# Optimization experiments

Hardware: AMD Instinct MI355X
Metric: run time of the kernel (lower is better)

## Reference

```python
import jax, jax.numpy as jnp
import numpy as np


def _quat_raw_mul(a, b):
    aw, ax, ay, az = a[..., 0], a[..., 1], a[..., 2], a[..., 3]
    bw, bx, by, bz = b[..., 0], b[..., 1], b[..., 2], b[..., 3]
    ow = aw * bw - ax * bx - ay * by - az * bz
    ox = aw * bx + ax * bw + ay * bz - az * by
    oy = aw * by - ax * bz + ay * bw + az * bx
    oz = aw * bz + ax * by - ay * bx + az * bw
    return jnp.stack([ow, ox, oy, oz], axis=-1)


def _standardize(q):
    # pytorch3d.quaternion_multiply standardizes sign so w >= 0
    return jnp.where(q[..., :1] < 0, -q, q)


def _quat_apply(q, v):
    # rotate points v by unit quaternions q: q * (0, v) * conj(q), take imaginary part
    pv = jnp.concatenate([jnp.zeros_like(v[..., :1]), v], axis=-1)
    conj = q * jnp.asarray([1.0, -1.0, -1.0, -1.0], dtype=q.dtype)
    return _quat_raw_mul(_quat_raw_mul(q, pv), conj)[..., 1:]


def _axis_angle_to_quat(aa):
    # pytorch3d.axis_angle_to_quaternion with small-angle Taylor branch
    angle = jnp.linalg.norm(aa, axis=-1, keepdims=True)
    half = 0.5 * angle
    eps = 1e-6
    small = jnp.abs(angle) < eps
    safe_angle = jnp.where(small, jnp.ones_like(angle), angle)
    k = jnp.where(small, 0.5 - angle * angle / 48.0, jnp.sin(half) / safe_angle)
    return jnp.concatenate([jnp.cos(half), aa * k], axis=-1)


def _matrix_to_quat(M):
    # pytorch3d.matrix_to_quaternion (candidate-selection form), vectorized
    m00, m11, m22 = M[..., 0, 0], M[..., 1, 1], M[..., 2, 2]
    q_abs = jnp.sqrt(jax.nn.relu(jnp.stack([
        1.0 + m00 + m11 + m22,
        1.0 + m00 - m11 - m22,
        1.0 - m00 + m11 - m22,
        1.0 - m00 - m11 + m22], axis=-1)))
    c0 = jnp.stack([q_abs[..., 0] ** 2, M[..., 2, 1] - M[..., 1, 2], M[..., 0, 2] - M[..., 2, 0], M[..., 1, 0] - M[..., 0, 1]], axis=-1)
    c1 = jnp.stack([M[..., 2, 1] - M[..., 1, 2], q_abs[..., 1] ** 2, M[..., 1, 0] + M[..., 0, 1], M[..., 0, 2] + M[..., 2, 0]], axis=-1)
    c2 = jnp.stack([M[..., 0, 2] - M[..., 2, 0], M[..., 1, 0] + M[..., 0, 1], q_abs[..., 2] ** 2, M[..., 2, 1] + M[..., 1, 2]], axis=-1)
    c3 = jnp.stack([M[..., 1, 0] - M[..., 0, 1], M[..., 2, 0] + M[..., 0, 2], M[..., 2, 1] + M[..., 1, 2], q_abs[..., 3] ** 2], axis=-1)
    cands = jnp.stack([c0, c1, c2, c3], axis=-2)  # (..., 4 candidates, 4)
    flr = 0.1
    cands = cands / (2.0 * jnp.maximum(q_abs[..., None], flr))
    idx = jnp.argmax(q_abs, axis=-1)
    return jnp.take_along_axis(cands, idx[..., None, None], axis=-2)[..., 0, :]


def _or6d_to_quat(d6):
    a1, a2 = d6[..., :3], d6[..., 3:]
    b1 = a1 / jnp.linalg.norm(a1, axis=-1, keepdims=True)
    a2p = a2 - jnp.sum(b1 * a2, axis=-1, keepdims=True) * b1
    b2 = a2p / jnp.linalg.norm(a2p, axis=-1, keepdims=True)
    b3 = jnp.cross(b1, b2)
    M = jnp.stack([b1, b2, b3], axis=-2)  # (..., 3, 3)
    return _matrix_to_quat(M)


def setup_inputs() -> dict:
    key = jax.random.key(0)
    k1, k2, k3, k4 = jax.random.split(key, 4)
    N, T, J = 256, 1024, 24
    return {
        'root_rvel': jax.random.normal(k1, (N, T, 1, 1), dtype=jnp.float32),
        'local_pos': jax.random.normal(k2, (N, T + 1, J, 3), dtype=jnp.float32),
        'local_rot': jax.random.normal(k3, (N, T + 1, J, 6), dtype=jnp.float32),
        'root_vel': jax.random.normal(k4, (N, T, 1, 2), dtype=jnp.float32),
    }


def reference(root_rvel, local_pos, local_rot, root_vel):
    # cumulative root yaw angle with zero initial frame: (N, T+1, 1, 1)
    r = jnp.cumsum(root_rvel, axis=1)
    r = jnp.concatenate([jnp.zeros_like(r[:, :1]), r], axis=1)
    # axis-angle about Y axis -> quaternion (N, T+1, 1, 4)
    aa = r * jnp.asarray([0.0, 1.0, 0.0], dtype=r.dtype)
    rotation = _axis_angle_to_quat(aa)
    # local 6D rotations -> quaternions (N, T+1, J, 4)
    local_q = _or6d_to_quat(local_rot)
    global_rot = _standardize(_quat_raw_mul(rotation, local_q))
    relative_pos = _quat_apply(rotation, local_pos)
    # lift XZ hip velocity to 3D, rotate into world frame, integrate
    zeros_y = jnp.zeros_like(root_vel[..., :1])
    v3 = jnp.concatenate([root_vel[..., :1], zeros_y, root_vel[..., 1:]], axis=-1)  # (N,T,1,3)
    v3w = _quat_apply(rotation[:, :-1], v3)
    pos_xz = jnp.concatenate([jnp.zeros_like(v3w[:, :1]), jnp.cumsum(v3w, axis=1)], axis=1)  # (N,T+1,1,3)
    global_pos = relative_pos + pos_xz
    return global_pos, global_rot
```

## Files before the change

### kernel.cpp

```cpp
#include <hip/hip_runtime.h>

#define N_SEQ 256
#define T_LEN 1024
#define TP1   (T_LEN + 1)
#define J_NUM 24
#define SEQ_ITEMS (TP1 * J_NUM)
#define TOTAL_ITEMS (N_SEQ * SEQ_ITEMS)
#define GP_TOTAL (N_SEQ * TP1 * J_NUM * 3)

#define IPB 512
#define NBLOCKS_B (TOTAL_ITEMS / IPB)

__device__ __forceinline__ float block_scan_incl(float v, float* wsum, int tid) {
    const int lane = tid & 63;
    const int wid  = tid >> 6;
    #pragma unroll
    for (int off = 1; off < 64; off <<= 1) {
        float u = __shfl_up(v, off, 64);
        if (lane >= off) v += u;
    }
    if (lane == 63) wsum[wid] = v;
    __syncthreads();
    if (tid == 0) {
        float acc = 0.0f;
        #pragma unroll
        for (int i = 0; i < 16; ++i) { float t = wsum[i]; wsum[i] = acc; acc += t; }
    }
    __syncthreads();
    return v + wsum[wid];
}

extern "C" __global__ void __launch_bounds__(1024)
scan_kernel(const float* __restrict__ root_rvel,
            const float* __restrict__ root_vel,
            float4* __restrict__ ws4)
{
    const int n   = blockIdx.x;
    const int tid = threadIdx.x;

    __shared__ float  r_s[TP1];
    __shared__ float2 quat_s[TP1];
    __shared__ float  ws_a[16], ws_b[16], ws_c[16];

    {
        float v = root_rvel[n * T_LEN + tid];
        float incl = block_scan_incl(v, ws_a, tid);
        if (tid == 0) r_s[0] = 0.0f;
        r_s[tid + 1] = incl;
    }
    __syncthreads();

    for (int idx = tid; idx < TP1; idx += 1024) {
        float r     = r_s[idx];
        float angle = fabsf(r);
        float half  = 0.5f * angle;
        float k = (angle < 1e-6f) ? (0.5f - angle * angle * (1.0f / 48.0f))
                                  : (__builtin_sinf(half) / angle);
        quat_s[idx] = make_float2(__builtin_cosf(half), r * k);
    }
    __syncthreads();

    {
        float2 vel = ((const float2*)root_vel)[n * T_LEN + tid];
        float2 q   = quat_s[tid];
        float  w = q.x, y = q.y;
        float t1x = w * vel.x + y * vel.y;
        float t1z = w * vel.y - y * vel.x;
        float ax  = t1x * w + t1z * y;
        float az  = t1z * w - t1x * y;
        float ix = block_scan_incl(ax, ws_b, tid);
        float iz = block_scan_incl(az, ws_c, tid);
        float2 qn = quat_s[tid + 1];
        ws4[n * TP1 + tid + 1] = make_float4(qn.x, qn.y, ix, iz);
        if (tid == 0) ws4[n * TP1] = make_float4(1.0f, 0.0f, 0.0f, 0.0f);
    }
}

__device__ __forceinline__ void process_item(
    float a1x, float a1y, float a1z, float a2x, float a2y, float a2z,
    float vx,  float vy,  float vz,  float4 wq,
    float4* __restrict__ out_rot_addr, float* __restrict__ s_out3)
{
    const float w = wq.x, yq = wq.y;

    float inv1 = __builtin_amdgcn_rsqf(a1x * a1x + a1y * a1y + a1z * a1z);
    float b1x = a1x * inv1, b1y = a1y * inv1, b1z = a1z * inv1;
    float dp  = b1x * a2x + b1y * a2y + b1z * a2z;
    float px  = a2x - dp * b1x, py = a2y - dp * b1y, pz = a2z - dp * b1z;
    float inv2 = __builtin_amdgcn_rsqf(px * px + py * py + pz * pz);
    float b2x = px * inv2, b2y = py * inv2, b2z = pz * inv2;
    float b3x = b1y * b2z - b1z * b2y;
    float b3y = b1z * b2x - b1x * b2z;
    float b3z = b1x * b2y - b1y * b2x;

    float m00 = b1x, m01 = b1y, m02 = b1z;
    float m10 = b2x, m11 = b2y, m12 = b2z;
    float m20 = b3x, m21 = b3y, m22 = b3z;

    float s0 = 1.0f + m00 + m11 + m22;
    float s1 = 1.0f + m00 - m11 - m22;
    float s2 = 1.0f - m00 + m11 - m22;
    float s3 = 1.0f - m00 - m11 + m22;

    int best = 0; float bs = s0;
    if (s1 > bs) { best = 1; bs = s1; }
    if (s2 > bs) { best = 2; bs = s2; }
    if (s3 > bs) { best = 3; bs = s3; }

    float c0 = m21 - m12, c1 = m02 - m20, c2 = m10 - m01;
    float d0 = m10 + m01, d1 = m02 + m20, d2 = m21 + m12;

    float lw = best == 0 ? bs : (best == 1 ? c0 : (best == 2 ? c1 : c2));
    float lx = best == 0 ? c0 : (best == 1 ? bs : (best == 2 ? d0 : d1));
    float ly = best == 0 ? c1 : (best == 1 ? d0 : (best == 2 ? bs : d2));
    float lz = best == 0 ? c2 : (best == 1 ? d1 : (best == 2 ? d2 : bs));

    float invd = __builtin_amdgcn_rcpf(2.0f * __builtin_amdgcn_sqrtf(bs));
    lw *= invd; lx *= invd; ly *= invd; lz *= invd;

    float ow = w * lw - yq * ly;
    float ox = w * lx + yq * lz;
    float oy = w * ly + yq * lw;
    float oz = w * lz - yq * lx;
    if (ow < 0.0f) { ow = -ow; ox = -ox; oy = -oy; oz = -oz; }
    *out_rot_addr = make_float4(ow, ox, oy, oz);

    float t1x = w * vx + yq * vz;
    float t1z = w * vz - yq * vx;
    s_out3[0] = t1x * w + t1z * yq + wq.z;
    s_out3[1] = (w * w + yq * yq) * vy;
    s_out3[2] = t1z * w - t1x * yq + wq.w;
}

extern "C" __global__ void __launch_bounds__(256, 8)
elem_kernel(const float4* __restrict__ rot4,
            const float4* __restrict__ pos4,
            const float4* __restrict__ ws4,
            float4* __restrict__ out_rot4,
            float4* __restrict__ out_pos4)
{
    __shared__ float4 s_rot4[768];
    __shared__ float4 s_pos4[384];
    float* s_rot = (float*)s_rot4;
    float* s_pos = (float*)s_pos4;
    float*  s_out  = s_rot;
    float4* s_out4 = s_rot4;

    const int tid = threadIdx.x;
    const unsigned blk = blockIdx.x;

    {
        const float4* rb = rot4 + (size_t)blk * 768;
        s_rot4[tid]       = rb[tid];
        s_rot4[tid + 256] = rb[tid + 256];
        s_rot4[tid + 512] = rb[tid + 512];
        const float4* pb = pos4 + (size_t)blk * 384;
        s_pos4[tid] = pb[tid];
        if (tid < 128) s_pos4[tid + 256] = pb[tid + 256];
    }

    const unsigned a0 = blk * (unsigned)IPB + (unsigned)tid;
    const unsigned a1 = a0 + 256u;
    const unsigned seq0 = a0 / (unsigned)SEQ_ITEMS;
    const unsigned t0   = (a0 - seq0 * (unsigned)SEQ_ITEMS) / (unsigned)J_NUM;
    const unsigned seq1 = a1 / (unsigned)SEQ_ITEMS;
    const unsigned t1   = (a1 - seq1 * (unsigned)SEQ_ITEMS) / (unsigned)J_NUM;
    const float4 wq0 = ws4[seq0 * (unsigned)TP1 + t0];
    const float4 wq1 = ws4[seq1 * (unsigned)TP1 + t1];

    __syncthreads();

    const float2* s_rot2 = (const float2*)s_rot;
    const int L0 = tid, L1 = tid + 256;
    float2 ra0 = s_rot2[3 * L0 + 0];
    float2 rb0 = s_rot2[3 * L0 + 1];
    float2 rc0 = s_rot2[3 * L0 + 2];
    float2 ra1 = s_rot2[3 * L1 + 0];
    float2 rb1 = s_rot2[3 * L1 + 1];
    float2 rc1 = s_rot2[3 * L1 + 2];
    float p0x = s_pos[3 * L0 + 0], p0y = s_pos[3 * L0 + 1], p0z = s_pos[3 * L0 + 2];
    float p1x = s_pos[3 * L1 + 0], p1y = s_pos[3 * L1 + 1], p1z = s_pos[3 * L1 + 2];

    __syncthreads();

    process_item(ra0.x, ra0.y, rb0.x, rb0.y, rc0.x, rc0.y,
                 p0x, p0y, p0z, wq0, &out_rot4[a0], &s_out[3 * L0]);
    process_item(ra1.x, ra1.y, rb1.x, rb1.y, rc1.x, rc1.y,
                 p1x, p1y, p1z, wq1, &out_rot4[a1], &s_out[3 * L1]);

    __syncthreads();

    float4* opb = out_pos4 + (size_t)blk * 384;
    opb[tid] = s_out4[tid];
    if (tid < 128) opb[tid + 256] = s_out4[tid + 256];
}

extern "C" void kernel_launch(void* const* d_in, const int* in_sizes, int n_in,
                              void* d_out, int out_size, void* d_ws, size_t ws_size,
                              hipStream_t stream) {
    (void)in_sizes; (void)n_in; (void)ws_size; (void)out_size;
    const float* root_rvel = (const float*)d_in[0];
    const float* local_pos = (const float*)d_in[1];
    const float* local_rot = (const float*)d_in[2];
    const float* root_vel  = (const float*)d_in[3];
    float* out = (float*)d_out;

    float4* ws4 = (float4*)d_ws;

    scan_kernel<<<N_SEQ, 1024, 0, stream>>>(root_rvel, root_vel, ws4);

    elem_kernel<<<NBLOCKS_B, 256, 0, stream>>>(
        (const float4*)local_rot, (const float4*)local_pos, ws4,
        (float4*)(out + GP_TOTAL),
        (float4*)out);
}
```

Before: 340.6 us.

## Convert elem kernel to persistent grid with register prefetch and nontemporal stores

Replaces the one-block-per-tile elem launch with a fixed grid of 1536 persistent blocks that loop over tiles. Each block prefetches the next tile's rotation, position and scan data into registers while computing the current tile. Outputs are written with nontemporal stores, and a separate shared output buffer is added so the prefetched data never overwrites the output staging. The aim is to overlap global loads with compute and keep writes from polluting cache, at the cost of more registers (launch bound lowered to 6 waves) and extra shared memory.

```diff
diff --git a/kernel.cpp b/kernel.cpp
--- a/kernel.cpp
+++ b/kernel.cpp
@@ -9,7 +9,15 @@
 #define GP_TOTAL (N_SEQ * TP1 * J_NUM * 3)
 
 #define IPB 512
-#define NBLOCKS_B (TOTAL_ITEMS / IPB)
+#define NTILES (TOTAL_ITEMS / IPB)
+#define PGRID 1536
+
+typedef float nfloat4 __attribute__((ext_vector_type(4)));
+
+__device__ __forceinline__ void nt_store4(float4 v, float4* p) {
+    nfloat4 nv = {v.x, v.y, v.z, v.w};
+    __builtin_nontemporal_store(nv, (nfloat4*)p);
+}
 
 __device__ __forceinline__ float block_scan_incl(float v, float* wsum, int tid) {
     const int lane = tid & 63;
@@ -123,7 +131,7 @@
     float oy = w * ly + yq * lw;
     float oz = w * lz - yq * lx;
     if (ow < 0.0f) { ow = -ow; ox = -ox; oy = -oy; oz = -oz; }
-    *out_rot_addr = make_float4(ow, ox, oy, oz);
+    nt_store4(make_float4(ow, ox, oy, oz), out_rot_addr);
 
     float t1x = w * vx + yq * vz;
     float t1z = w * vz - yq * vx;
@@ -132,7 +140,7 @@
     s_out3[2] = t1z * w - t1x * yq + wq.w;
 }
 
-extern "C" __global__ void __launch_bounds__(256, 8)
+extern "C" __global__ void __launch_bounds__(256, 6)
 elem_kernel(const float4* __restrict__ rot4,
             const float4* __restrict__ pos4,
             const float4* __restrict__ ws4,
@@ -141,58 +149,84 @@
 {
     __shared__ float4 s_rot4[768];
     __shared__ float4 s_pos4[384];
+    __shared__ float4 s_out4[384];
     float* s_rot = (float*)s_rot4;
     float* s_pos = (float*)s_pos4;
-    float*  s_out  = s_rot;
-    float4* s_out4 = s_rot4;
+    float* s_out = (float*)s_out4;
 
     const int tid = threadIdx.x;
-    const unsigned blk = blockIdx.x;
+    unsigned tile = blockIdx.x;
+
+    float4 nr0, nr1, nr2, np0, np1, nwq0, nwq1;
 
     {
-        const float4* rb = rot4 + (size_t)blk * 768;
-        s_rot4[tid]       = rb[tid];
-        s_rot4[tid + 256] = rb[tid + 256];
-        s_rot4[tid + 512] = rb[tid + 512];
-        const float4* pb = pos4 + (size_t)blk * 384;
-        s_pos4[tid] = pb[tid];
-        if (tid < 128) s_pos4[tid + 256] = pb[tid + 256];
-    }
-
-    const unsigned a0 = blk * (unsigned)IPB + (unsigned)tid;
-    const unsigned a1 = a0 + 256u;
-    const unsigned seq0 = a0 / (unsigned)SEQ_ITEMS;
-    const unsigned t0   = (a0 - seq0 * (unsigned)SEQ_ITEMS) / (unsigned)J_NUM;
-    const unsigned seq1 = a1 / (unsigned)SEQ_ITEMS;
-    const unsigned t1   = (a1 - seq1 * (unsigned)SEQ_ITEMS) / (unsigned)J_NUM;
-    const float4 wq0 = ws4[seq0 * (unsigned)TP1 + t0];
-    const float4 wq1 = ws4[seq1 * (unsigned)TP1 + t1];
-
-    __syncthreads();
-
-    const float2* s_rot2 = (const float2*)s_rot;
-    const int L0 = tid, L1 = tid + 256;
-    float2 ra0 = s_rot2[3 * L0 + 0];
-    float2 rb0 = s_rot2[3 * L0 + 1];
-    float2 rc0 = s_rot2[3 * L0 + 2];
-    float2 ra1 = s_rot2[3 * L1 + 0];
-    float2 rb1 = s_rot2[3 * L1 + 1];
-    float2 rc1 = s_rot2[3 * L1 + 2];
-    float p0x = s_pos[3 * L0 + 0], p0y = s_pos[3 * L0 + 1], p0z = s_pos[3 * L0 + 2];
-    float p1x = s_pos[3 * L1 + 0], p1y = s_pos[3 * L1 + 1], p1z = s_pos[3 * L1 + 2];
-
-    __syncthreads();
-
-    process_item(ra0.x, ra0.y, rb0.x, rb0.y, rc0.x, rc0.y,
-                 p0x, p0y, p0z, wq0, &out_rot4[a0], &s_out[3 * L0]);
-    process_item(ra1.x, ra1.y, rb1.x, rb1.y, rc1.x, rc1.y,
-                 p1x, p1y, p1z, wq1, &out_rot4[a1], &s_out[3 * L1]);
-
-    __syncthreads();
-
-    float4* opb = out_pos4 + (size_t)blk * 384;
-    opb[tid] = s_out4[tid];
-    if (tid < 128) opb[tid + 256] = s_out4[tid + 256];
+        const float4* rb = rot4 + (size_t)tile * 768;
+        nr0 = rb[tid]; nr1 = rb[tid + 256]; nr2 = rb[tid + 512];
+        const float4* pb = pos4 + (size_t)tile * 384;
+        np0 = pb[tid];
+        np1 = (tid < 128) ? pb[tid + 256] : make_float4(0.f, 0.f, 0.f, 0.f);
+        unsigned a0 = tile * (unsigned)IPB + (unsigned)tid, a1 = a0 + 256u;
+        unsigned q0 = a0 / (unsigned)SEQ_ITEMS, t0 = (a0 - q0 * (unsigned)SEQ_ITEMS) / (unsigned)J_NUM;
+        unsigned q1 = a1 / (unsigned)SEQ_ITEMS, t1 = (a1 - q1 * (unsigned)SEQ_ITEMS) / (unsigned)J_NUM;
+        nwq0 = ws4[q0 * (unsigned)TP1 + t0];
+        nwq1 = ws4[q1 * (unsigned)TP1 + t1];
+    }
+    s_rot4[tid] = nr0; s_rot4[tid + 256] = nr1; s_rot4[tid + 512] = nr2;
+    s_pos4[tid] = np0; if (tid < 128) s_pos4[tid + 256] = np1;
+    float4 cwq0 = nwq0, cwq1 = nwq1;
+    __syncthreads();
+
+    for (;;) {
+        const unsigned next = tile + (unsigned)PGRID;
+        const bool has = next < (unsigned)NTILES;
+
+        if (has) {
+            const float4* rb = rot4 + (size_t)next * 768;
+            nr0 = rb[tid]; nr1 = rb[tid + 256]; nr2 = rb[tid + 512];
+            const float4* pb = pos4 + (size_t)next * 384;
+            np0 = pb[tid];
+            if (tid < 128) np1 = pb[tid + 256];
+            unsigned a0 = next * (unsigned)IPB + (unsigned)tid, a1 = a0 + 256u;
+            unsigned q0 = a0 / (unsigned)SEQ_ITEMS, t0 = (a0 - q0 * (unsigned)SEQ_ITEMS) / (unsigned)J_NUM;
+            unsigned q1 = a1 / (unsigned)SEQ_ITEMS, t1 = (a1 - q1 * (unsigned)SEQ_ITEMS) / (unsigned)J_NUM;
+            nwq0 = ws4[q0 * (unsigned)TP1 + t0];
+            nwq1 = ws4[q1 * (unsigned)TP1 + t1];
+        }
+
+        {
+            const unsigned a0 = tile * (unsigned)IPB + (unsigned)tid;
+            const unsigned a1 = a0 + 256u;
+            const float2* s_rot2 = (const float2*)s_rot;
+            const int L0 = tid, L1 = tid + 256;
+            float2 ra0 = s_rot2[3 * L0 + 0];
+            float2 rb0 = s_rot2[3 * L0 + 1];
+            float2 rc0 = s_rot2[3 * L0 + 2];
+            float2 ra1 = s_rot2[3 * L1 + 0];
+            float2 rb1 = s_rot2[3 * L1 + 1];
+            float2 rc1 = s_rot2[3 * L1 + 2];
+            float p0x = s_pos[3 * L0 + 0], p0y = s_pos[3 * L0 + 1], p0z = s_pos[3 * L0 + 2];
+            float p1x = s_pos[3 * L1 + 0], p1y = s_pos[3 * L1 + 1], p1z = s_pos[3 * L1 + 2];
+
+            process_item(ra0.x, ra0.y, rb0.x, rb0.y, rc0.x, rc0.y,
+                         p0x, p0y, p0z, cwq0, &out_rot4[a0], &s_out[3 * L0]);
+            process_item(ra1.x, ra1.y, rb1.x, rb1.y, rc1.x, rc1.y,
+                         p1x, p1y, p1z, cwq1, &out_rot4[a1], &s_out[3 * L1]);
+        }
+
+        __syncthreads();
+
+        {
+            float4* opb = out_pos4 + (size_t)tile * 384;
+            nt_store4(s_out4[tid], &opb[tid]);
+            if (tid < 128) nt_store4(s_out4[tid + 256], &opb[tid + 256]);
+        }
+        if (!has) break;
+        s_rot4[tid] = nr0; s_rot4[tid + 256] = nr1; s_rot4[tid + 512] = nr2;
+        s_pos4[tid] = np0; if (tid < 128) s_pos4[tid + 256] = np1;
+        cwq0 = nwq0; cwq1 = nwq1;
+        __syncthreads();
+        tile = next;
+    }
 }
 
 extern "C" void kernel_launch(void* const* d_in, const int* in_sizes, int n_in,
@@ -209,7 +243,7 @@
 
     scan_kernel<<<N_SEQ, 1024, 0, stream>>>(root_rvel, root_vel, ws4);
 
-    elem_kernel<<<NBLOCKS_B, 256, 0, stream>>>(
+    elem_kernel<<<PGRID, 256, 0, stream>>>(
         (const float4*)local_rot, (const float4*)local_pos, ws4,
         (float4*)(out + GP_TOTAL),
         (float4*)out);
```

Measured after the change: 353.0 us. +3.6%, slower.
